# Optimization experiments

Measured on AMD Instinct MI355X. Metric: run time of the kernel, lower is better.

Reference implementation:

```python
import jax, jax.numpy as jnp
import numpy as np

N_NODES = 100000
N_EDGES = 1600000
N_GRAPHS = 512
IN_DIM, HID, GOUT, SCAL = 256, 128, 64, 2


def setup_inputs() -> dict:
    key = jax.random.key(0)
    ks = jax.random.split(key, 12)
    x = jax.random.normal(ks[0], (N_NODES, IN_DIM), dtype=jnp.float32)
    edge_index = jax.random.randint(ks[1], (2, N_EDGES), 0, N_NODES, dtype=jnp.int64)
    batch = jnp.sort(jax.random.randint(ks[2], (N_NODES,), 0, N_GRAPHS, dtype=jnp.int64))
    scalars = jax.random.normal(ks[3], (N_GRAPHS, SCAL), dtype=jnp.float32)
    def lin(k, fan_in, fan_out):
        s = 1.0 / np.sqrt(fan_in)
        kw, kb = jax.random.split(k)
        W = jax.random.uniform(kw, (fan_in, fan_out), minval=-s, maxval=s, dtype=jnp.float32)
        b = jax.random.uniform(kb, (fan_out,), minval=-s, maxval=s, dtype=jnp.float32)
        return W, b
    W1, b1 = lin(ks[4], IN_DIM, HID)
    W2, b2 = lin(ks[5], HID, GOUT)
    W3, b3 = lin(ks[6], GOUT + SCAL, HID)
    W4, b4 = lin(ks[7], HID, 1)
    return {"x": x, "edge_index": edge_index, "batch": batch, "scalars": scalars,
            "W1": W1, "b1": b1, "W2": W2, "b2": b2,
            "W3": W3, "b3": b3, "W4": W4, "b4": b4}


def gcn_conv(x, W, b, src, dst, num_nodes):
    # PyG GCNConv: h = x @ W; add self-loops; norm = d^-1/2[src] * d^-1/2[dst]
    # with deg = in-degree (on dst) + 1 (self-loop); scatter-add into dst.
    h = x @ W  # [N, F]
    deg = jax.ops.segment_sum(jnp.ones((src.shape[0],), h.dtype), dst,
                              num_segments=num_nodes) + 1.0
    dinv = jax.lax.rsqrt(deg)  # [N]
    norm = dinv[src] * dinv[dst]  # [E]
    agg = jax.ops.segment_sum(h[src] * norm[:, None], dst, num_segments=num_nodes)
    agg = agg + h * (dinv * dinv)[:, None]  # self-loop contribution
    return agg + b


def global_mean_pool(x, batch, num_graphs):
    s = jax.ops.segment_sum(x, batch, num_segments=num_graphs)
    cnt = jax.ops.segment_sum(jnp.ones((x.shape[0],), x.dtype), batch,
                              num_segments=num_graphs)
    return s / jnp.maximum(cnt, 1.0)[:, None]


def reference(x, edge_index, batch, scalars, W1, b1, W2, b2, W3, b3, W4, b4):
    src, dst = edge_index[0], edge_index[1]
    h = jax.nn.relu(gcn_conv(x, W1, b1, src, dst, N_NODES))
    h = gcn_conv(h, W2, b2, src, dst, N_NODES)
    emb = global_mean_pool(h, batch, N_GRAPHS)  # [G, GOUT]
    combined = jnp.concatenate([emb, scalars], axis=1)  # [G, GOUT+SCAL]
    out = jax.nn.sigmoid(jax.nn.relu(combined @ W3 + b3) @ W4 + b4)
    return out.reshape(-1, 1)
```

## Files before the change

### kernel.cpp

```cpp
#include <hip/hip_runtime.h>

#define NN 100000
#define NE 1600000
#define NG 512
#define NPARTS 500
#define PW 200
#define NCHUNKS 128
#define CE 12500
#define NCNT (NPARTS * NCHUNKS)

typedef unsigned int uint;
typedef unsigned short ushort;
typedef __bf16 bf16x8 __attribute__((ext_vector_type(8)));
typedef float f32x4 __attribute__((ext_vector_type(4)));

__device__ inline uint f2bf2(float a, float b) {
  uint ua = __float_as_uint(a), ub = __float_as_uint(b);
  ua += 0x7fff + ((ua >> 16) & 1);
  ub += 0x7fff + ((ub >> 16) & 1);
  return (ua >> 16) | (ub & 0xffff0000u);
}
__device__ inline ushort f2bf(float f) {
  uint u = __float_as_uint(f);
  u += 0x7fff + ((u >> 16) & 1);
  return (ushort)(u >> 16);
}
__device__ inline float2 bf2f(uint v) {
  float2 r;
  r.x = __uint_as_float(v << 16);
  r.y = __uint_as_float(v & 0xffff0000u);
  return r;
}
__device__ inline uint relu2(uint u) {
  uint lo = (u & 0x8000u) ? 0u : (u & 0xFFFFu);
  uint hi = (u & 0x80000000u) ? 0u : (u & 0xFFFF0000u);
  return lo | hi;
}

__global__ __launch_bounds__(256) void transpose_w2(const float* __restrict__ W1, uint* __restrict__ w1t,
                                                    const float* __restrict__ W2, uint* __restrict__ w2t) {
  __shared__ float col[256];
  int b = blockIdx.x, k = threadIdx.x;
  const float* W; uint* Wt; int K, N, n;
  if (b < 128) { W = W1; Wt = w1t; K = 256; N = 128; n = b; }
  else         { W = W2; Wt = w2t; K = 128; N = 64;  n = b - 128; }
  if (k < K) col[k] = W[(size_t)k * N + n];
  __syncthreads();
  if (k < K / 2) Wt[(size_t)n * (K / 2) + k] = f2bf2(col[2 * k], col[2 * k + 1]);
}

__global__ __launch_bounds__(256) void bucket_count(const int* __restrict__ dst,
                                                    int* __restrict__ cnt) {
  __shared__ int h[NPARTS];
  int t = threadIdx.x, c = blockIdx.x;
  for (int i = t; i < NPARTS; i += 256) h[i] = 0;
  __syncthreads();
  int beg = c * CE;
  for (int j = t; j < CE; j += 256) atomicAdd(&h[dst[beg + j] / PW], 1);
  __syncthreads();
  for (int i = t; i < NPARTS; i += 256) cnt[i * NCHUNKS + c] = h[i];
}

__global__ void scan1(const int* __restrict__ in, int* __restrict__ out,
                      int* __restrict__ bsum, int n) {
  __shared__ int s[256];
  int t = threadIdx.x;
  int i = blockIdx.x * 256 + t;
  int v = (i < n) ? in[i] : 0;
  s[t] = v;
  __syncthreads();
  for (int off = 1; off < 256; off <<= 1) {
    int add = (t >= off) ? s[t - off] : 0;
    __syncthreads();
    s[t] += add;
    __syncthreads();
  }
  if (i < n) out[i] = s[t] - v;
  if (t == 255) bsum[blockIdx.x] = s[255];
}

__global__ void scan2(int* __restrict__ bsum, int nb) {
  __shared__ int s[512];
  int t = threadIdx.x;
  int v = (t < nb) ? bsum[t] : 0;
  s[t] = v;
  __syncthreads();
  for (int off = 1; off < 512; off <<= 1) {
    int add = (t >= off) ? s[t - off] : 0;
    __syncthreads();
    s[t] += add;
    __syncthreads();
  }
  if (t < nb) bsum[t] = s[t] - v;
}

__global__ void scan3(int* __restrict__ out, const int* __restrict__ bsum, int n) {
  int i = blockIdx.x * 256 + threadIdx.x;
  if (i < n) out[i] += bsum[blockIdx.x];
}

__global__ __launch_bounds__(256) void bucket_scatter(const int* __restrict__ src,
                                                      const int* __restrict__ dst,
                                                      const int* __restrict__ off,
                                                      uint* __restrict__ pk) {
  __shared__ int cur[NPARTS];
  int t = threadIdx.x, c = blockIdx.x;
  for (int i = t; i < NPARTS; i += 256) cur[i] = off[i * NCHUNKS + c];
  __syncthreads();
  int beg = c * CE;
  for (int j = t; j < CE; j += 256) {
    int d = dst[beg + j];
    int p = d / PW;
    int pos = atomicAdd(&cur[p], 1);
    pk[pos] = (uint)src[beg + j] | ((uint)(d - p * PW) << 17);
  }
}

__global__ __launch_bounds__(256) void csr_finalize(const uint* __restrict__ pk,
                                                    const int* __restrict__ off,
                                                    int* __restrict__ row_off,
                                                    float* __restrict__ dinv,
                                                    int* __restrict__ csr) {
  __shared__ int hist[PW];
  __shared__ int cur[PW];
  __shared__ int s[256];
  int p = blockIdx.x, t = threadIdx.x;
  int base = off[p * NCHUNKS];
  int endp = (p == NPARTS - 1) ? NE : off[(p + 1) * NCHUNKS];
  if (t < PW) hist[t] = 0;
  __syncthreads();
  for (int j = base + t; j < endp; j += 256) atomicAdd(&hist[pk[j] >> 17], 1);
  __syncthreads();
  int v = (t < PW) ? hist[t] : 0;
  s[t] = v;
  __syncthreads();
  for (int o = 1; o < 256; o <<= 1) {
    int add = (t >= o) ? s[t - o] : 0;
    __syncthreads();
    s[t] += add;
    __syncthreads();
  }
  if (t < PW) {
    int excl = base + (s[t] - v);
    int node = p * PW + t;
    row_off[node] = excl;
    dinv[node]    = rsqrtf((float)v + 1.0f);
    cur[t] = excl;
  }
  if (p == NPARTS - 1 && t == 0) row_off[NN] = NE;
  __syncthreads();
  for (int j = base + t; j < endp; j += 256) {
    uint e = pk[j];
    int pos = atomicAdd(&cur[e >> 17], 1);
    csr[pos] = (int)(e & 0x1FFFFu);
  }
}

template<int K, int N, int WM, int WN, int A_BF16, int RELU>
__global__ __launch_bounds__(256) void gemm_direct(const void* __restrict__ Av,
                                                   const uint* __restrict__ Bt,
                                                   const float* __restrict__ dinv,
                                                   ushort* __restrict__ Cb, int M) {
  __shared__ __align__(16) char bsm[N * K * 2];
  const int tid  = threadIdx.x;
  const int wid  = tid >> 6;
  const int lane = tid & 63;
  const int wm   = wid % WM;
  const int wn   = wid / WM;
  const int l15  = lane & 15;
  const int lk   = lane >> 4;
  const int blockRow = blockIdx.x * (WM * 32);

  constexpr int UPR = K / 8;
  constexpr int TOT = N * K / 8;
#pragma unroll
  for (int i0 = 0; i0 < TOT; i0 += 256) {
    int i = i0 + tid;
    uint4 v = reinterpret_cast<const uint4*>(Bt)[i];
    int n = i / UPR, c = i % UPR;
    int byte = (n * (K * 2) + c * 16) ^ ((n & 7) << 4);
    *reinterpret_cast<uint4*>(bsm + byte) = v;
  }
  __syncthreads();

  f32x4 acc[2][4];
#pragma unroll
  for (int i = 0; i < 2; ++i)
#pragma unroll
    for (int j = 0; j < 4; ++j) acc[i][j] = (f32x4){0.f, 0.f, 0.f, 0.f};

#pragma unroll
  for (int kk = 0; kk < K / 32; ++kk) {
    bf16x8 af[2], bfr[4];
#pragma unroll
    for (int mt = 0; mt < 2; ++mt) {
      int grow = blockRow + wm * 32 + mt * 16 + l15;
      int row = grow < M ? grow : M - 1;
      if (A_BF16) {
        uint4 va = *reinterpret_cast<const uint4*>((const uint*)Av + (size_t)row * (K / 2) + kk * 16 + lk * 4);
        if (RELU) { va.x = relu2(va.x); va.y = relu2(va.y); va.z = relu2(va.z); va.w = relu2(va.w); }
        af[mt] = __builtin_bit_cast(bf16x8, va);
      } else {
        const float4* p = reinterpret_cast<const float4*>((const float*)Av + (size_t)row * K + kk * 32 + lk * 8);
        float4 f0 = p[0], f1 = p[1];
        uint4 va;
        va.x = f2bf2(f0.x, f0.y); va.y = f2bf2(f0.z, f0.w);
        va.z = f2bf2(f1.x, f1.y); va.w = f2bf2(f1.z, f1.w);
        af[mt] = __builtin_bit_cast(bf16x8, va);
      }
    }
#pragma unroll
    for (int nt = 0; nt < 4; ++nt) {
      int n = wn * 64 + nt * 16 + l15;
      int byte = (n * (K * 2) + kk * 64 + lk * 16) ^ ((n & 7) << 4);
      bfr[nt] = __builtin_bit_cast(bf16x8, *reinterpret_cast<uint4*>(bsm + byte));
    }
#pragma unroll
    for (int mt = 0; mt < 2; ++mt)
#pragma unroll
      for (int nt = 0; nt < 4; ++nt)
        acc[mt][nt] = __builtin_amdgcn_mfma_f32_16x16x32_bf16(af[mt], bfr[nt], acc[mt][nt], 0, 0, 0);
  }

#pragma unroll
  for (int mt = 0; mt < 2; ++mt) {
    int rbase = blockRow + wm * 32 + mt * 16 + lk * 4;
#pragma unroll
    for (int j = 0; j < 4; ++j) {
      int grow = rbase + j;
      if (grow < M) {
        float d = dinv[grow];
#pragma unroll
        for (int nt = 0; nt < 4; ++nt) {
          int gcol = wn * 64 + nt * 16 + l15;
          Cb[(size_t)grow * N + gcol] = f2bf(acc[mt][nt][j] * d);
        }
      }
    }
  }
}

__global__ __launch_bounds__(256) void agg_csr_f128_v2(const uint4* __restrict__ hs,
                                                       const float* __restrict__ dinv,
                                                       const float* __restrict__ bias,
                                                       const int* __restrict__ row_off,
                                                       const int* __restrict__ csr,
                                                       uint4* __restrict__ outb, int N) {
  int node = blockIdx.x * 4 + (threadIdx.x >> 6);
  if (node >= N) return;
  int lane = threadIdx.x & 63;
  int sl = lane >> 4;
  int c4 = lane & 15;
  int beg = row_off[node], end = row_off[node + 1];
  float a0=0,a1=0,a2=0,a3=0,a4=0,a5=0,a6=0,a7=0;
  int j = beg;
  for (; j + 16 <= end; j += 16) {
    int s0 = csr[j + sl];
    int s1 = csr[j + 4 + sl];
    int s2 = csr[j + 8 + sl];
    int s3 = csr[j + 12 + sl];
    uint4 v0 = hs[(size_t)s0 * 16 + c4];
    uint4 v1 = hs[(size_t)s1 * 16 + c4];
    uint4 v2 = hs[(size_t)s2 * 16 + c4];
    uint4 v3 = hs[(size_t)s3 * 16 + c4];
    float2 f;
    f = bf2f(v0.x); a0+=f.x; a1+=f.y;  f = bf2f(v0.y); a2+=f.x; a3+=f.y;
    f = bf2f(v0.z); a4+=f.x; a5+=f.y;  f = bf2f(v0.w); a6+=f.x; a7+=f.y;
    f = bf2f(v1.x); a0+=f.x; a1+=f.y;  f = bf2f(v1.y); a2+=f.x; a3+=f.y;
    f = bf2f(v1.z); a4+=f.x; a5+=f.y;  f = bf2f(v1.w); a6+=f.x; a7+=f.y;
    f = bf2f(v2.x); a0+=f.x; a1+=f.y;  f = bf2f(v2.y); a2+=f.x; a3+=f.y;
    f = bf2f(v2.z); a4+=f.x; a5+=f.y;  f = bf2f(v2.w); a6+=f.x; a7+=f.y;
    f = bf2f(v3.x); a0+=f.x; a1+=f.y;  f = bf2f(v3.y); a2+=f.x; a3+=f.y;
    f = bf2f(v3.z); a4+=f.x; a5+=f.y;  f = bf2f(v3.w); a6+=f.x; a7+=f.y;
  }
  for (; j + 4 <= end; j += 4) {
    int s0 = csr[j + sl];
    uint4 v0 = hs[(size_t)s0 * 16 + c4];
    float2 f;
    f = bf2f(v0.x); a0+=f.x; a1+=f.y;  f = bf2f(v0.y); a2+=f.x; a3+=f.y;
    f = bf2f(v0.z); a4+=f.x; a5+=f.y;  f = bf2f(v0.w); a6+=f.x; a7+=f.y;
  }
  if (j + sl < end) {
    int s0 = csr[j + sl];
    uint4 v0 = hs[(size_t)s0 * 16 + c4];
    float2 f;
    f = bf2f(v0.x); a0+=f.x; a1+=f.y;  f = bf2f(v0.y); a2+=f.x; a3+=f.y;
    f = bf2f(v0.z); a4+=f.x; a5+=f.y;  f = bf2f(v0.w); a6+=f.x; a7+=f.y;
  }
  a0 += __shfl_xor(a0, 16); a1 += __shfl_xor(a1, 16); a2 += __shfl_xor(a2, 16); a3 += __shfl_xor(a3, 16);
  a4 += __shfl_xor(a4, 16); a5 += __shfl_xor(a5, 16); a6 += __shfl_xor(a6, 16); a7 += __shfl_xor(a7, 16);
  a0 += __shfl_xor(a0, 32); a1 += __shfl_xor(a1, 32); a2 += __shfl_xor(a2, 32); a3 += __shfl_xor(a3, 32);
  a4 += __shfl_xor(a4, 32); a5 += __shfl_xor(a5, 32); a6 += __shfl_xor(a6, 32); a7 += __shfl_xor(a7, 32);
  if (sl == 0) {
    uint4 v = hs[(size_t)node * 16 + c4];
    float2 f;
    f = bf2f(v.x); a0+=f.x; a1+=f.y;  f = bf2f(v.y); a2+=f.x; a3+=f.y;
    f = bf2f(v.z); a4+=f.x; a5+=f.y;  f = bf2f(v.w); a6+=f.x; a7+=f.y;
    float d = dinv[node];
    const float4* bp = reinterpret_cast<const float4*>(bias);
    float4 b0 = bp[c4 * 2], b1 = bp[c4 * 2 + 1];
    uint4 o;
    o.x = f2bf2(fmaf(a0, d, b0.x), fmaf(a1, d, b0.y));
    o.y = f2bf2(fmaf(a2, d, b0.z), fmaf(a3, d, b0.w));
    o.z = f2bf2(fmaf(a4, d, b1.x), fmaf(a5, d, b1.y));
    o.w = f2bf2(fmaf(a6, d, b1.z), fmaf(a7, d, b1.w));
    outb[(size_t)node * 16 + c4] = o;
  }
}

__global__ __launch_bounds__(256) void agg_csr_f64_v2(const uint4* __restrict__ hs,
                                                      const float* __restrict__ dinv,
                                                      const int* __restrict__ row_off,
                                                      const int* __restrict__ csr,
                                                      float* __restrict__ out, int N) {
  int node = blockIdx.x * 4 + (threadIdx.x >> 6);
  if (node >= N) return;
  int lane = threadIdx.x & 63;
  int sl = lane >> 3;
  int c4 = lane & 7;
  int beg = row_off[node], end = row_off[node + 1];
  float a0=0,a1=0,a2=0,a3=0,a4=0,a5=0,a6=0,a7=0;
  int j = beg;
  for (; j + 16 <= end; j += 16) {
    int s0 = csr[j + sl];
    int s1 = csr[j + 8 + sl];
    uint4 v0 = hs[(size_t)s0 * 8 + c4];
    uint4 v1 = hs[(size_t)s1 * 8 + c4];
    float2 f;
    f = bf2f(v0.x); a0+=f.x; a1+=f.y;  f = bf2f(v0.y); a2+=f.x; a3+=f.y;
    f = bf2f(v0.z); a4+=f.x; a5+=f.y;  f = bf2f(v0.w); a6+=f.x; a7+=f.y;
    f = bf2f(v1.x); a0+=f.x; a1+=f.y;  f = bf2f(v1.y); a2+=f.x; a3+=f.y;
    f = bf2f(v1.z); a4+=f.x; a5+=f.y;  f = bf2f(v1.w); a6+=f.x; a7+=f.y;
  }
  for (; j + 8 <= end; j += 8) {
    int s0 = csr[j + sl];
    uint4 v0 = hs[(size_t)s0 * 8 + c4];
    float2 f;
    f = bf2f(v0.x); a0+=f.x; a1+=f.y;  f = bf2f(v0.y); a2+=f.x; a3+=f.y;
    f = bf2f(v0.z); a4+=f.x; a5+=f.y;  f = bf2f(v0.w); a6+=f.x; a7+=f.y;
  }
  if (j + sl < end) {
    int s0 = csr[j + sl];
    uint4 v0 = hs[(size_t)s0 * 8 + c4];
    float2 f;
    f = bf2f(v0.x); a0+=f.x; a1+=f.y;  f = bf2f(v0.y); a2+=f.x; a3+=f.y;
    f = bf2f(v0.z); a4+=f.x; a5+=f.y;  f = bf2f(v0.w); a6+=f.x; a7+=f.y;
  }
  a0 += __shfl_xor(a0, 8);  a1 += __shfl_xor(a1, 8);  a2 += __shfl_xor(a2, 8);  a3 += __shfl_xor(a3, 8);
  a4 += __shfl_xor(a4, 8);  a5 += __shfl_xor(a5, 8);  a6 += __shfl_xor(a6, 8);  a7 += __shfl_xor(a7, 8);
  a0 += __shfl_xor(a0, 16); a1 += __shfl_xor(a1, 16); a2 += __shfl_xor(a2, 16); a3 += __shfl_xor(a3, 16);
  a4 += __shfl_xor(a4, 16); a5 += __shfl_xor(a5, 16); a6 += __shfl_xor(a6, 16); a7 += __shfl_xor(a7, 16);
  a0 += __shfl_xor(a0, 32); a1 += __shfl_xor(a1, 32); a2 += __shfl_xor(a2, 32); a3 += __shfl_xor(a3, 32);
  a4 += __shfl_xor(a4, 32); a5 += __shfl_xor(a5, 32); a6 += __shfl_xor(a6, 32); a7 += __shfl_xor(a7, 32);
  if (sl == 0) {
    uint4 v = hs[(size_t)node * 8 + c4];
    float2 f;
    f = bf2f(v.x); a0+=f.x; a1+=f.y;  f = bf2f(v.y); a2+=f.x; a3+=f.y;
    f = bf2f(v.z); a4+=f.x; a5+=f.y;  f = bf2f(v.w); a6+=f.x; a7+=f.y;
    float d = dinv[node];
    float4 o0 = make_float4(a0 * d, a1 * d, a2 * d, a3 * d);
    float4 o1 = make_float4(a4 * d, a5 * d, a6 * d, a7 * d);
    float4* op = reinterpret_cast<float4*>(out + (size_t)node * 64 + c4 * 8);
    op[0] = o0;
    op[1] = o1;
  }
}

__global__ __launch_bounds__(256) void pool_graph(const float* __restrict__ h,
                                                  const int* __restrict__ batch,
                                                  const float* __restrict__ scalars,
                                                  float* __restrict__ emb66, int N) {
  int g = blockIdx.x;
  int t = threadIdx.x;
  int col = t & 63, rr = t >> 6;
  __shared__ int range[2];
  __shared__ float part[4][64];
  if (t < 2) {
    int target = g + t;
    int lo = 0, hi = N;
    while (lo < hi) { int mid = (lo + hi) >> 1; if (batch[mid] < target) lo = mid + 1; else hi = mid; }
    range[t] = lo;
  }
  __syncthreads();
  int beg = range[0], end = range[1];
  float s = 0.f;
  for (int i = beg + rr; i < end; i += 4) s += h[(size_t)i * 64 + col];
  part[rr][col] = s;
  __syncthreads();
  if (rr == 0) {
    float tot = (part[0][col] + part[1][col]) + (part[2][col] + part[3][col]);
    emb66[g * 66 + col] = tot / fmaxf((float)(end - beg), 1.f);
  } else if (t >= 64 && t < 66) {
    emb66[g * 66 + t] = scalars[g * 2 + (t - 64)];
  }
}

__global__ __launch_bounds__(128) void graph_mlp3(const float* __restrict__ emb66,
                                                  const float* __restrict__ b2,
                                                  const float* __restrict__ W3,
                                                  const float* __restrict__ b3,
                                                  const float* __restrict__ W4,
                                                  const float* __restrict__ b4,
                                                  float* __restrict__ out) {
  int g = blockIdx.x;
  int t = threadIdx.x;
  __shared__ float comb[66];
  __shared__ float part[2];
  if (t < 64)      comb[t] = emb66[g * 66 + t] + b2[t];
  else if (t < 66) comb[t] = emb66[g * 66 + t];
  __syncthreads();
  float h = b3[t];
#pragma unroll
  for (int k = 0; k < 66; ++k) h += comb[k] * W3[k * 128 + t];
  h = fmaxf(h, 0.f);
  float p = h * W4[t];
#pragma unroll
  for (int off = 32; off > 0; off >>= 1) p += __shfl_down(p, off);
  if ((t & 63) == 0) part[t >> 6] = p;
  __syncthreads();
  if (t == 0) {
    float s = part[0] + part[1] + b4[0];
    out[g] = 1.f / (1.f + expf(-s));
  }
}

extern "C" void kernel_launch(void* const* d_in, const int* in_sizes, int n_in,
                              void* d_out, int out_size, void* d_ws, size_t ws_size,
                              hipStream_t stream) {
  const float* x       = (const float*)d_in[0];
  const int*   ei      = (const int*)d_in[1];
  const int*   src     = ei;
  const int*   dstp    = ei + NE;
  const int*   batch   = (const int*)d_in[2];
  const float* scalars = (const float*)d_in[3];
  const float* W1 = (const float*)d_in[4];  const float* b1 = (const float*)d_in[5];
  const float* W2 = (const float*)d_in[6];  const float* b2 = (const float*)d_in[7];
  const float* W3 = (const float*)d_in[8];  const float* b3 = (const float*)d_in[9];
  const float* W4 = (const float*)d_in[10]; const float* b4 = (const float*)d_in[11];
  float* out = (float*)d_out;

  uint*  ws      = (uint*)d_ws;
  uint*  w1t     = ws;
  uint*  w2t     = ws + 16384;
  uint*  hsb     = ws + 20480;
  uint*  agg1b   = hsb + 6400000;
  float* dinv    = (float*)(agg1b + 6400000);
  int*   row_off = (int*)(dinv + NN);
  int*   csr     = row_off + NN + 4;
  uint*  pk      = (uint*)(csr + NE);
  int*   cnt     = (int*)(pk + NE);
  int*   bsum    = cnt + NCNT;
  float* emb66   = (float*)(bsum + 512);

  bucket_count<<<NCHUNKS, 256, 0, stream>>>(dstp, cnt);
  scan1<<<(NCNT + 255) / 256, 256, 0, stream>>>(cnt, cnt, bsum, NCNT);
  scan2<<<1, 512, 0, stream>>>(bsum, (NCNT + 255) / 256);
  scan3<<<(NCNT + 255) / 256, 256, 0, stream>>>(cnt, bsum, NCNT);
  bucket_scatter<<<NCHUNKS, 256, 0, stream>>>(src, dstp, cnt, pk);
  csr_finalize<<<NPARTS, 256, 0, stream>>>(pk, cnt, row_off, dinv, csr);

  transpose_w2<<<192, 256, 0, stream>>>(W1, w1t, W2, w2t);

  gemm_direct<256, 128, 2, 2, 0, 0><<<(NN + 63) / 64, 256, 0, stream>>>(
      x, w1t, dinv, (ushort*)hsb, NN);
  agg_csr_f128_v2<<<(NN + 3) / 4, 256, 0, stream>>>((const uint4*)hsb, dinv, b1,
                                                    row_off, csr, (uint4*)agg1b, NN);

  gemm_direct<128, 64, 4, 1, 1, 1><<<(NN + 127) / 128, 256, 0, stream>>>(
      agg1b, w2t, dinv, (ushort*)hsb, NN);
  agg_csr_f64_v2<<<(NN + 3) / 4, 256, 0, stream>>>((const uint4*)hsb, dinv,
                                                   row_off, csr, (float*)agg1b, NN);

  pool_graph<<<NG, 256, 0, stream>>>((const float*)agg1b, batch, scalars, emb66, NN);
  graph_mlp3<<<NG, 128, 0, stream>>>(emb66, b2, W3, b3, W4, b4, out);
}
```

Measured before the change: 251.3 us.

## Fuse prep kernels, fold scan offsets into consumers, fuse pool+MLP, retile GEMM1

Merges the weight transpose and bucket counting into one launch, removes the scan3 pass by adding block sums inside bucket_scatter and csr_finalize, and fuses mean pooling with the graph MLP. The first GEMM is retiled to 4x1 warps with 128-row blocks and a templated N-tile count. The goal is fewer kernel launches and less intermediate traffic. In exchange the first GEMM keeps more accumulator registers per warp, with 8 N-tiles instead of 4.

Result: faster. 233.2 us (-7.2%).

```diff
diff --git a/kernel.cpp b/kernel.cpp
--- a/kernel.cpp
+++ b/kernel.cpp
@@ -37,28 +37,28 @@
   return lo | hi;
 }
 
-__global__ __launch_bounds__(256) void transpose_w2(const float* __restrict__ W1, uint* __restrict__ w1t,
-                                                    const float* __restrict__ W2, uint* __restrict__ w2t) {
-  __shared__ float col[256];
-  int b = blockIdx.x, k = threadIdx.x;
-  const float* W; uint* Wt; int K, N, n;
-  if (b < 128) { W = W1; Wt = w1t; K = 256; N = 128; n = b; }
-  else         { W = W2; Wt = w2t; K = 128; N = 64;  n = b - 128; }
-  if (k < K) col[k] = W[(size_t)k * N + n];
-  __syncthreads();
-  if (k < K / 2) Wt[(size_t)n * (K / 2) + k] = f2bf2(col[2 * k], col[2 * k + 1]);
-}
-
-__global__ __launch_bounds__(256) void bucket_count(const int* __restrict__ dst,
-                                                    int* __restrict__ cnt) {
-  __shared__ int h[NPARTS];
-  int t = threadIdx.x, c = blockIdx.x;
-  for (int i = t; i < NPARTS; i += 256) h[i] = 0;
-  __syncthreads();
-  int beg = c * CE;
-  for (int j = t; j < CE; j += 256) atomicAdd(&h[dst[beg + j] / PW], 1);
-  __syncthreads();
-  for (int i = t; i < NPARTS; i += 256) cnt[i * NCHUNKS + c] = h[i];
+__global__ __launch_bounds__(256) void prep(const float* __restrict__ W1, uint* __restrict__ w1t,
+                                            const float* __restrict__ W2, uint* __restrict__ w2t,
+                                            const int* __restrict__ dst, int* __restrict__ cnt) {
+  int b = blockIdx.x, t = threadIdx.x;
+  if (b < 192) {
+    __shared__ float col[256];
+    const float* W; uint* Wt; int K, N, n;
+    if (b < 128) { W = W1; Wt = w1t; K = 256; N = 128; n = b; }
+    else         { W = W2; Wt = w2t; K = 128; N = 64;  n = b - 128; }
+    if (t < K) col[t] = W[(size_t)t * N + n];
+    __syncthreads();
+    if (t < K / 2) Wt[(size_t)n * (K / 2) + t] = f2bf2(col[2 * t], col[2 * t + 1]);
+  } else {
+    __shared__ int h[NPARTS];
+    int c = b - 192;
+    for (int i = t; i < NPARTS; i += 256) h[i] = 0;
+    __syncthreads();
+    int beg = c * CE;
+    for (int j = t; j < CE; j += 256) atomicAdd(&h[dst[beg + j] / PW], 1);
+    __syncthreads();
+    for (int i = t; i < NPARTS; i += 256) cnt[i * NCHUNKS + c] = h[i];
+  }
 }
 
 __global__ void scan1(const int* __restrict__ in, int* __restrict__ out,
@@ -94,18 +94,17 @@
   if (t < nb) bsum[t] = s[t] - v;
 }
 
-__global__ void scan3(int* __restrict__ out, const int* __restrict__ bsum, int n) {
-  int i = blockIdx.x * 256 + threadIdx.x;
-  if (i < n) out[i] += bsum[blockIdx.x];
-}
-
 __global__ __launch_bounds__(256) void bucket_scatter(const int* __restrict__ src,
                                                       const int* __restrict__ dst,
                                                       const int* __restrict__ off,
+                                                      const int* __restrict__ bsum,
                                                       uint* __restrict__ pk) {
   __shared__ int cur[NPARTS];
   int t = threadIdx.x, c = blockIdx.x;
-  for (int i = t; i < NPARTS; i += 256) cur[i] = off[i * NCHUNKS + c];
+  for (int i = t; i < NPARTS; i += 256) {
+    int idx = i * NCHUNKS + c;
+    cur[i] = off[idx] + bsum[idx >> 8];
+  }
   __syncthreads();
   int beg = c * CE;
   for (int j = t; j < CE; j += 256) {
@@ -118,6 +117,7 @@
 
 __global__ __launch_bounds__(256) void csr_finalize(const uint* __restrict__ pk,
                                                     const int* __restrict__ off,
+                                                    const int* __restrict__ bsum,
                                                     int* __restrict__ row_off,
                                                     float* __restrict__ dinv,
                                                     int* __restrict__ csr) {
@@ -125,8 +125,13 @@
   __shared__ int cur[PW];
   __shared__ int s[256];
   int p = blockIdx.x, t = threadIdx.x;
-  int base = off[p * NCHUNKS];
-  int endp = (p == NPARTS - 1) ? NE : off[(p + 1) * NCHUNKS];
+  int idx0 = p * NCHUNKS;
+  int base = off[idx0] + bsum[idx0 >> 8];
+  int endp = NE;
+  if (p < NPARTS - 1) {
+    int idx1 = (p + 1) * NCHUNKS;
+    endp = off[idx1] + bsum[idx1 >> 8];
+  }
   if (t < PW) hist[t] = 0;
   __syncthreads();
   for (int j = base + t; j < endp; j += 256) atomicAdd(&hist[pk[j] >> 17], 1);
@@ -161,6 +166,8 @@
                                                    const uint* __restrict__ Bt,
                                                    const float* __restrict__ dinv,
                                                    ushort* __restrict__ Cb, int M) {
+  constexpr int NW = N / WN;
+  constexpr int NT = NW / 16;
   __shared__ __align__(16) char bsm[N * K * 2];
   const int tid  = threadIdx.x;
   const int wid  = tid >> 6;
@@ -183,15 +190,15 @@
   }
   __syncthreads();
 
-  f32x4 acc[2][4];
+  f32x4 acc[2][NT];
 #pragma unroll
   for (int i = 0; i < 2; ++i)
 #pragma unroll
-    for (int j = 0; j < 4; ++j) acc[i][j] = (f32x4){0.f, 0.f, 0.f, 0.f};
+    for (int j = 0; j < NT; ++j) acc[i][j] = (f32x4){0.f, 0.f, 0.f, 0.f};
 
 #pragma unroll
   for (int kk = 0; kk < K / 32; ++kk) {
-    bf16x8 af[2], bfr[4];
+    bf16x8 af[2], bfr[NT];
 #pragma unroll
     for (int mt = 0; mt < 2; ++mt) {
       int grow = blockRow + wm * 32 + mt * 16 + l15;
@@ -210,15 +217,15 @@
       }
     }
 #pragma unroll
-    for (int nt = 0; nt < 4; ++nt) {
-      int n = wn * 64 + nt * 16 + l15;
+    for (int nt = 0; nt < NT; ++nt) {
+      int n = wn * NW + nt * 16 + l15;
       int byte = (n * (K * 2) + kk * 64 + lk * 16) ^ ((n & 7) << 4);
       bfr[nt] = __builtin_bit_cast(bf16x8, *reinterpret_cast<uint4*>(bsm + byte));
     }
 #pragma unroll
     for (int mt = 0; mt < 2; ++mt)
 #pragma unroll
-      for (int nt = 0; nt < 4; ++nt)
+      for (int nt = 0; nt < NT; ++nt)
         acc[mt][nt] = __builtin_amdgcn_mfma_f32_16x16x32_bf16(af[mt], bfr[nt], acc[mt][nt], 0, 0, 0);
   }
 
@@ -231,8 +238,8 @@
       if (grow < M) {
         float d = dinv[grow];
 #pragma unroll
-        for (int nt = 0; nt < 4; ++nt) {
-          int gcol = wn * 64 + nt * 16 + l15;
+        for (int nt = 0; nt < NT; ++nt) {
+          int gcol = wn * NW + nt * 16 + l15;
           Cb[(size_t)grow * N + gcol] = f2bf(acc[mt][nt][j] * d);
         }
       }
@@ -366,15 +373,22 @@
   }
 }
 
-__global__ __launch_bounds__(256) void pool_graph(const float* __restrict__ h,
-                                                  const int* __restrict__ batch,
-                                                  const float* __restrict__ scalars,
-                                                  float* __restrict__ emb66, int N) {
+__global__ __launch_bounds__(256) void pool_mlp(const float* __restrict__ h,
+                                                const int* __restrict__ batch,
+                                                const float* __restrict__ scalars,
+                                                const float* __restrict__ b2,
+                                                const float* __restrict__ W3,
+                                                const float* __restrict__ b3,
+                                                const float* __restrict__ W4,
+                                                const float* __restrict__ b4,
+                                                float* __restrict__ out, int N) {
   int g = blockIdx.x;
   int t = threadIdx.x;
   int col = t & 63, rr = t >> 6;
   __shared__ int range[2];
   __shared__ float part[4][64];
+  __shared__ float comb[66];
+  __shared__ float red[2];
   if (t < 2) {
     int target = g + t;
     int lo = 0, hi = N;
@@ -389,38 +403,25 @@
   __syncthreads();
   if (rr == 0) {
     float tot = (part[0][col] + part[1][col]) + (part[2][col] + part[3][col]);
-    emb66[g * 66 + col] = tot / fmaxf((float)(end - beg), 1.f);
-  } else if (t >= 64 && t < 66) {
-    emb66[g * 66 + t] = scalars[g * 2 + (t - 64)];
-  }
-}
-
-__global__ __launch_bounds__(128) void graph_mlp3(const float* __restrict__ emb66,
-                                                  const float* __restrict__ b2,
-                                                  const float* __restrict__ W3,
-                                                  const float* __restrict__ b3,
-                                                  const float* __restrict__ W4,
-                                                  const float* __restrict__ b4,
-                                                  float* __restrict__ out) {
-  int g = blockIdx.x;
-  int t = threadIdx.x;
-  __shared__ float comb[66];
-  __shared__ float part[2];
-  if (t < 64)      comb[t] = emb66[g * 66 + t] + b2[t];
-  else if (t < 66) comb[t] = emb66[g * 66 + t];
-  __syncthreads();
-  float h = b3[t];
-#pragma unroll
-  for (int k = 0; k < 66; ++k) h += comb[k] * W3[k * 128 + t];
-  h = fmaxf(h, 0.f);
-  float p = h * W4[t];
-#pragma unroll
-  for (int off = 32; off > 0; off >>= 1) p += __shfl_down(p, off);
-  if ((t & 63) == 0) part[t >> 6] = p;
+    comb[col] = tot / fmaxf((float)(end - beg), 1.f) + b2[col];
+  } else if (t == 64 || t == 65) {
+    comb[t] = scalars[g * 2 + (t - 64)];
+  }
+  __syncthreads();
+  if (t < 128) {
+    float hh = b3[t];
+#pragma unroll
+    for (int k = 0; k < 66; ++k) hh += comb[k] * W3[k * 128 + t];
+    hh = fmaxf(hh, 0.f);
+    float p = hh * W4[t];
+#pragma unroll
+    for (int off = 32; off > 0; off >>= 1) p += __shfl_down(p, off);
+    if ((t & 63) == 0) red[t >> 6] = p;
+  }
   __syncthreads();
   if (t == 0) {
-    float s = part[0] + part[1] + b4[0];
-    out[g] = 1.f / (1.f + expf(-s));
+    float sum = red[0] + red[1] + b4[0];
+    out[g] = 1.f / (1.f + expf(-sum));
   }
 }
 
@@ -450,18 +451,15 @@
   uint*  pk      = (uint*)(csr + NE);
   int*   cnt     = (int*)(pk + NE);
   int*   bsum    = cnt + NCNT;
-  float* emb66   = (float*)(bsum + 512);
-
-  bucket_count<<<NCHUNKS, 256, 0, stream>>>(dstp, cnt);
+
+  prep<<<320, 256, 0, stream>>>(W1, w1t, W2, w2t, dstp, cnt);
+
   scan1<<<(NCNT + 255) / 256, 256, 0, stream>>>(cnt, cnt, bsum, NCNT);
   scan2<<<1, 512, 0, stream>>>(bsum, (NCNT + 255) / 256);
-  scan3<<<(NCNT + 255) / 256, 256, 0, stream>>>(cnt, bsum, NCNT);
-  bucket_scatter<<<NCHUNKS, 256, 0, stream>>>(src, dstp, cnt, pk);
-  csr_finalize<<<NPARTS, 256, 0, stream>>>(pk, cnt, row_off, dinv, csr);
-
-  transpose_w2<<<192, 256, 0, stream>>>(W1, w1t, W2, w2t);
-
-  gemm_direct<256, 128, 2, 2, 0, 0><<<(NN + 63) / 64, 256, 0, stream>>>(
+  bucket_scatter<<<NCHUNKS, 256, 0, stream>>>(src, dstp, cnt, bsum, pk);
+  csr_finalize<<<NPARTS, 256, 0, stream>>>(pk, cnt, bsum, row_off, dinv, csr);
+
+  gemm_direct<256, 128, 4, 1, 0, 0><<<(NN + 127) / 128, 256, 0, stream>>>(
       x, w1t, dinv, (ushort*)hsb, NN);
   agg_csr_f128_v2<<<(NN + 3) / 4, 256, 0, stream>>>((const uint4*)hsb, dinv, b1,
                                                     row_off, csr, (uint4*)agg1b, NN);
@@ -471,6 +469,6 @@
   agg_csr_f64_v2<<<(NN + 3) / 4, 256, 0, stream>>>((const uint4*)hsb, dinv,
                                                    row_off, csr, (float*)agg1b, NN);
 
-  pool_graph<<<NG, 256, 0, stream>>>((const float*)agg1b, batch, scalars, emb66, NN);
-  graph_mlp3<<<NG, 128, 0, stream>>>(emb66, b2, W3, b3, W4, b4, out);
-}
+  pool_mlp<<<NG, 256, 0, stream>>>((const float*)agg1b, batch, scalars, b2,
+                                   W3, b3, W4, b4, out, NN);
+}
```
